# Kernel optimization log

Hardware: AMD Instinct MI355X
Metric: run time of the kernel (lower is better)

The kernel has to match this reference:

```python
import jax, jax.numpy as jnp
import numpy as np

N_ITER = 50  # entmax_bisect default number of bisection iterations
ALPHA_MIN = 1.001


def setup_inputs() -> dict:
    key = jax.random.key(0)
    k1, k2 = jax.random.split(key)
    B, S = 4096, 4096
    scores = jax.random.normal(k1, (B, S), dtype=jnp.float32)
    mask = jax.random.randint(k2, (B, S), 0, 2).astype(bool)  # True = keep
    alpha = jnp.array(1.5, dtype=jnp.float32)  # learned scalar parameter
    return {"scores": scores, "mask": mask, "alpha": alpha}


def _entmax_bisect(Xs, alpha, n_iter=N_ITER):
    """Xs: scores already multiplied by (alpha-1), masked positions = -inf.
    Bisection search for the threshold tau such that sum(clip(Xs-tau,0)^(1/(alpha-1))) = 1.
    """
    d = Xs.shape[-1]
    exp = 1.0 / (alpha - 1.0)

    def p_of(tau):  # elementwise (clip(Xs - tau, 0))**exp, grad-safe at 0
        z = Xs - tau
        z_safe = jnp.where(z > 0, z, 1.0)
        return jnp.where(z > 0, z_safe ** exp, 0.0)

    max_val = jnp.max(Xs, axis=-1, keepdims=True)
    tau_lo = max_val - 1.0                                   # _gp(1, alpha) = 1
    tau_hi = max_val - (1.0 / d) ** (alpha - 1.0)            # _gp(1/d, alpha)
    f_lo = jnp.sum(p_of(tau_lo), axis=-1, keepdims=True) - 1.0  # fixed across iterations
    dm0 = tau_hi - tau_lo
    p0 = p_of(tau_lo)

    def body(carry, _):
        tau_lo, dm, _p = carry
        dm = dm * 0.5
        tau_m = tau_lo + dm
        p_m = p_of(tau_m)
        f_m = jnp.sum(p_m, axis=-1, keepdims=True) - 1.0
        tau_lo = jnp.where(f_m * f_lo >= 0, tau_m, tau_lo)
        return (tau_lo, dm, p_m), None

    (_, _, p_m), _ = jax.lax.scan(body, (tau_lo, dm0, p0), None, length=n_iter)
    # ensure_sum_one=True in entmax_bisect
    return p_m / jnp.sum(p_m, axis=-1, keepdims=True)


def reference(scores, mask, alpha):
    alpha_c = jnp.maximum(alpha, ALPHA_MIN)  # torch clamps alpha.data to >= 1.001
    # replace_masked_values(scores, mask, -inf), then X * (alpha - 1)
    Xs = jnp.where(mask, scores * (alpha_c - 1.0), -jnp.inf)
    return _entmax_bisect(Xs, alpha_c)
```

## Files before the change

### kernel.cpp

```cpp
#include <hip/hip_runtime.h>

#define DLEN     4096
#define TPB      256
#define NWAVE    4
#define EPT      16
#define CAPW     1024
#define AS_MAX    6
#define NBISECT  31

typedef float floatx4 __attribute__((ext_vector_type(4)));

__device__ __forceinline__ int prefix_cnt(unsigned long long bm) {
    return __builtin_amdgcn_mbcnt_hi((unsigned)(bm >> 32),
           __builtin_amdgcn_mbcnt_lo((unsigned)bm, 0u));
}

__global__ __launch_bounds__(TPB, 8)
void entmax_kernel(const float* __restrict__ scores,
                   const int* __restrict__ mask,
                   const float* __restrict__ alpha_ptr,
                   float* __restrict__ out)
{
    __shared__ float sv[NWAVE][CAPW + 64];
    __shared__ int   wcnt[NWAVE];
    __shared__ float wred[NWAVE];

    const int tid  = threadIdx.x;
    const int w    = tid >> 6;
    const int lane = tid & 63;
    const int row  = blockIdx.x;

    const float NEG = -1e30f;

    const float alpha = fmaxf(alpha_ptr[0], 1.001f);
    const float am1   = alpha - 1.0f;
    const float expo  = 1.0f / am1;
    const bool  sq    = (expo == 2.0f);

    const size_t base = (size_t)row * DLEN;
    const float* srow = scores + base;
    const int*   mrow = mask + base;

    float xs[EPT];
    float wmax = NEG;
#pragma unroll
    for (int c = 0; c < 4; ++c) {
        const int idx = c * (TPB * 4) + tid * 4;
        const float4 s = *reinterpret_cast<const float4*>(srow + idx);
        const int4   m = *reinterpret_cast<const int4*>(mrow + idx);
        const float x0 = m.x ? s.x * am1 : NEG;
        const float x1 = m.y ? s.y * am1 : NEG;
        const float x2 = m.z ? s.z * am1 : NEG;
        const float x3 = m.w ? s.w * am1 : NEG;
        xs[c*4+0] = x0; xs[c*4+1] = x1; xs[c*4+2] = x2; xs[c*4+3] = x3;
        wmax = fmaxf(wmax, fmaxf(fmaxf(x0, x1), fmaxf(x2, x3)));
    }
#pragma unroll
    for (int off = 32; off; off >>= 1)
        wmax = fmaxf(wmax, __shfl_xor(wmax, off));
    if (lane == 0) wred[w] = wmax;
    __syncthreads();
    const float rmax = fmaxf(fmaxf(wred[0], wred[1]), fmaxf(wred[2], wred[3]));

    const float tau_lo0 = rmax - 1.0f;

    int cnt = 0;
#pragma unroll
    for (int e = 0; e < EPT; ++e) {
        const bool pred = xs[e] > tau_lo0;
        const unsigned long long bm = __ballot(pred);
        if (pred)
            sv[w][cnt + prefix_cnt(bm)] = xs[e];
        cnt += __popcll(bm);
    }
    sv[w][cnt + lane] = NEG;
    if (lane == 0) wcnt[w] = cnt;
    __syncthreads();

    int nct[NWAVE];
    bool fast = true;
#pragma unroll
    for (int ws = 0; ws < NWAVE; ++ws) {
        const int c4 = wcnt[ws];
        nct[ws] = (c4 + 63) >> 6;
        fast = fast && (c4 <= 64);
    }

    float tau_m = tau_lo0;
    float sum_m = 1.0f;

    if (sq) {
        float k_prev = -1.0f;
        if (fast) {
            const float r0 = sv[0][lane];
            const float r1 = sv[1][lane];
            const float r2 = sv[2][lane];
            const float r3 = sv[3][lane];
#pragma unroll 1
            for (int it = 0; it < AS_MAX; ++it) {
                const float z0 = fmaxf(r0 - tau_m, 0.f);
                const float z1 = fmaxf(r1 - tau_m, 0.f);
                const float z2 = fmaxf(r2 - tau_m, 0.f);
                const float z3 = fmaxf(r3 - tau_m, 0.f);
                float s2 = z0 * z0;
                s2 = fmaf(z1, z1, s2);
                s2 = fmaf(z2, z2, s2);
                s2 = fmaf(z3, z3, s2);
                float s1 = (z0 + z1) + (z2 + z3);
                float k  = ((z0 > 0.f ? 1.f : 0.f) + (z1 > 0.f ? 1.f : 0.f))
                         + ((z2 > 0.f ? 1.f : 0.f) + (z3 > 0.f ? 1.f : 0.f));
#pragma unroll
                for (int off = 32; off; off >>= 1) {
                    s2 += __shfl_xor(s2, off);
                    s1 += __shfl_xor(s1, off);
                    k  += __shfl_xor(k,  off);
                }
                sum_m = s2;
                if (k == k_prev || k <= 0.f) break;
                k_prev = k;
                const float disc = fmaxf(fmaf(-k, s2 - 1.0f, s1 * s1), 0.f);
                tau_m += (s1 - sqrtf(disc)) / k;
            }
        } else {
#pragma unroll 1
            for (int it = 0; it < AS_MAX; ++it) {
                float s2 = 0.f, s1 = 0.f, k = 0.f;
                for (int ws = 0; ws < NWAVE; ++ws) {
                    const int n = nct[ws];
                    for (int c = 0; c < n; ++c) {
                        const float z = fmaxf(sv[ws][c * 64 + lane] - tau_m, 0.f);
                        s2 = fmaf(z, z, s2);
                        s1 += z;
                        k  += (z > 0.f) ? 1.f : 0.f;
                    }
                }
#pragma unroll
                for (int off = 32; off; off >>= 1) {
                    s2 += __shfl_xor(s2, off);
                    s1 += __shfl_xor(s1, off);
                    k  += __shfl_xor(k,  off);
                }
                sum_m = s2;
                if (k == k_prev || k <= 0.f) break;
                k_prev = k;
                const float disc = fmaxf(fmaf(-k, s2 - 1.0f, s1 * s1), 0.f);
                tau_m += (s1 - sqrtf(disc)) / k;
            }
        }
    } else {
        const float tau_hi = rmax - exp2f(-12.0f * am1);

        auto rsum = [&](float tau) -> float {
            float s = 0.f;
            for (int ws = 0; ws < NWAVE; ++ws) {
                const int n = nct[ws];
                for (int c = 0; c < n; ++c) {
                    const float z = sv[ws][c * 64 + lane] - tau;
                    s += (z > 0.f) ? powf(z, expo) : 0.f;
                }
            }
#pragma unroll
            for (int off = 32; off; off >>= 1) s += __shfl_xor(s, off);
            return s;
        };

        float tau_lo = tau_lo0;
        const float f_lo = rsum(tau_lo0) - 1.0f;
        float dm = tau_hi - tau_lo0;
#pragma unroll 1
        for (int it = 0; it < NBISECT; ++it) {
            dm *= 0.5f;
            tau_m = tau_lo + dm;
            sum_m = rsum(tau_m);
            const float f_m = sum_m - 1.0f;
            tau_lo = (f_m * f_lo >= 0.0f) ? tau_m : tau_lo;
        }
    }

    const float inv = 1.0f / sum_m;
#pragma unroll
    for (int c = 0; c < 4; ++c) {
        const int idx = c * (TPB * 4) + tid * 4;
        floatx4 o;
        if (sq) {
            float z;
            z = fmaxf(xs[c*4+0] - tau_m, 0.f); o.x = z * z * inv;
            z = fmaxf(xs[c*4+1] - tau_m, 0.f); o.y = z * z * inv;
            z = fmaxf(xs[c*4+2] - tau_m, 0.f); o.z = z * z * inv;
            z = fmaxf(xs[c*4+3] - tau_m, 0.f); o.w = z * z * inv;
        } else {
            float z;
            z = xs[c*4+0] - tau_m; o.x = (z > 0.f) ? powf(z, expo) * inv : 0.f;
            z = xs[c*4+1] - tau_m; o.y = (z > 0.f) ? powf(z, expo) * inv : 0.f;
            z = xs[c*4+2] - tau_m; o.z = (z > 0.f) ? powf(z, expo) * inv : 0.f;
            z = xs[c*4+3] - tau_m; o.w = (z > 0.f) ? powf(z, expo) * inv : 0.f;
        }
        __builtin_nontemporal_store(o, reinterpret_cast<floatx4*>(out + base + idx));
    }
}

extern "C" void kernel_launch(void* const* d_in, const int* in_sizes, int n_in,
                              void* d_out, int out_size, void* d_ws, size_t ws_size,
                              hipStream_t stream) {
    const float* scores = (const float*)d_in[0];
    const int*   mask   = (const int*)d_in[1];
    const float* alpha  = (const float*)d_in[2];
    float*       out    = (float*)d_out;
    const int rows = in_sizes[0] / DLEN;
    entmax_kernel<<<rows, TPB, 0, stream>>>(scores, mask, alpha, out);
}
```

Before: 39.11 us.

## Process two rows per block and prefetch the next row during the solve

Each block now handles two consecutive rows. It issues the global loads for the next row's scores and mask into registers right after the compaction barrier, so they overlap the threshold solve and output store of the current row. The aim is to hide memory latency that was previously exposed at the start of each block. In exchange the grid is halved, which lowers parallelism across CUs, and the prefetch buffers raise register pressure under launch bounds of 8 blocks per CU. There is also a possible hazard on the shared buffers when the second row overwrites them.

```diff
diff --git a/kernel.cpp b/kernel.cpp
--- a/kernel.cpp
+++ b/kernel.cpp
@@ -3,6 +3,7 @@
 #define DLEN     4096
 #define TPB      256
 #define NWAVE    4
+#define RPB      2
 #define EPT      16
 #define CAPW     1024
 #define AS_MAX    6
@@ -19,7 +20,8 @@
 void entmax_kernel(const float* __restrict__ scores,
                    const int* __restrict__ mask,
                    const float* __restrict__ alpha_ptr,
-                   float* __restrict__ out)
+                   float* __restrict__ out,
+                   int rows)
 {
     __shared__ float sv[NWAVE][CAPW + 64];
     __shared__ int   wcnt[NWAVE];
@@ -28,7 +30,6 @@
     const int tid  = threadIdx.x;
     const int w    = tid >> 6;
     const int lane = tid & 63;
-    const int row  = blockIdx.x;
 
     const float NEG = -1e30f;
 
@@ -37,165 +38,194 @@
     const float expo  = 1.0f / am1;
     const bool  sq    = (expo == 2.0f);
 
-    const size_t base = (size_t)row * DLEN;
-    const float* srow = scores + base;
-    const int*   mrow = mask + base;
-
-    float xs[EPT];
-    float wmax = NEG;
-#pragma unroll
-    for (int c = 0; c < 4; ++c) {
-        const int idx = c * (TPB * 4) + tid * 4;
-        const float4 s = *reinterpret_cast<const float4*>(srow + idx);
-        const int4   m = *reinterpret_cast<const int4*>(mrow + idx);
-        const float x0 = m.x ? s.x * am1 : NEG;
-        const float x1 = m.y ? s.y * am1 : NEG;
-        const float x2 = m.z ? s.z * am1 : NEG;
-        const float x3 = m.w ? s.w * am1 : NEG;
-        xs[c*4+0] = x0; xs[c*4+1] = x1; xs[c*4+2] = x2; xs[c*4+3] = x3;
-        wmax = fmaxf(wmax, fmaxf(fmaxf(x0, x1), fmaxf(x2, x3)));
+    const int row0 = blockIdx.x * RPB;
+
+    float4 s_pf[4];
+    int4   m_pf[4];
+
+    {
+        const float* srow = scores + (size_t)row0 * DLEN;
+        const int*   mrow = mask   + (size_t)row0 * DLEN;
+#pragma unroll
+        for (int c = 0; c < 4; ++c) {
+            const int idx = c * (TPB * 4) + tid * 4;
+            s_pf[c] = *reinterpret_cast<const float4*>(srow + idx);
+            m_pf[c] = *reinterpret_cast<const int4*>(mrow + idx);
+        }
     }
-#pragma unroll
-    for (int off = 32; off; off >>= 1)
-        wmax = fmaxf(wmax, __shfl_xor(wmax, off));
-    if (lane == 0) wred[w] = wmax;
-    __syncthreads();
-    const float rmax = fmaxf(fmaxf(wred[0], wred[1]), fmaxf(wred[2], wred[3]));
-
-    const float tau_lo0 = rmax - 1.0f;
-
-    int cnt = 0;
-#pragma unroll
-    for (int e = 0; e < EPT; ++e) {
-        const bool pred = xs[e] > tau_lo0;
-        const unsigned long long bm = __ballot(pred);
-        if (pred)
-            sv[w][cnt + prefix_cnt(bm)] = xs[e];
-        cnt += __popcll(bm);
-    }
-    sv[w][cnt + lane] = NEG;
-    if (lane == 0) wcnt[w] = cnt;
-    __syncthreads();
-
-    int nct[NWAVE];
-    bool fast = true;
-#pragma unroll
-    for (int ws = 0; ws < NWAVE; ++ws) {
-        const int c4 = wcnt[ws];
-        nct[ws] = (c4 + 63) >> 6;
-        fast = fast && (c4 <= 64);
-    }
-
-    float tau_m = tau_lo0;
-    float sum_m = 1.0f;
-
-    if (sq) {
-        float k_prev = -1.0f;
-        if (fast) {
-            const float r0 = sv[0][lane];
-            const float r1 = sv[1][lane];
-            const float r2 = sv[2][lane];
-            const float r3 = sv[3][lane];
-#pragma unroll 1
-            for (int it = 0; it < AS_MAX; ++it) {
-                const float z0 = fmaxf(r0 - tau_m, 0.f);
-                const float z1 = fmaxf(r1 - tau_m, 0.f);
-                const float z2 = fmaxf(r2 - tau_m, 0.f);
-                const float z3 = fmaxf(r3 - tau_m, 0.f);
-                float s2 = z0 * z0;
-                s2 = fmaf(z1, z1, s2);
-                s2 = fmaf(z2, z2, s2);
-                s2 = fmaf(z3, z3, s2);
-                float s1 = (z0 + z1) + (z2 + z3);
-                float k  = ((z0 > 0.f ? 1.f : 0.f) + (z1 > 0.f ? 1.f : 0.f))
-                         + ((z2 > 0.f ? 1.f : 0.f) + (z3 > 0.f ? 1.f : 0.f));
-#pragma unroll
-                for (int off = 32; off; off >>= 1) {
-                    s2 += __shfl_xor(s2, off);
-                    s1 += __shfl_xor(s1, off);
-                    k  += __shfl_xor(k,  off);
+
+#pragma unroll 1
+    for (int r = 0; r < RPB; ++r) {
+        const int row = row0 + r;
+        if (row >= rows) break;
+        const size_t base = (size_t)row * DLEN;
+
+        float xs[EPT];
+        float wmax = NEG;
+#pragma unroll
+        for (int c = 0; c < 4; ++c) {
+            const float4 s = s_pf[c];
+            const int4   m = m_pf[c];
+            const float x0 = m.x ? s.x * am1 : NEG;
+            const float x1 = m.y ? s.y * am1 : NEG;
+            const float x2 = m.z ? s.z * am1 : NEG;
+            const float x3 = m.w ? s.w * am1 : NEG;
+            xs[c*4+0] = x0; xs[c*4+1] = x1; xs[c*4+2] = x2; xs[c*4+3] = x3;
+            wmax = fmaxf(wmax, fmaxf(fmaxf(x0, x1), fmaxf(x2, x3)));
+        }
+#pragma unroll
+        for (int off = 32; off; off >>= 1)
+            wmax = fmaxf(wmax, __shfl_xor(wmax, off));
+        if (lane == 0) wred[w] = wmax;
+        __syncthreads();
+        const float rmax = fmaxf(fmaxf(wred[0], wred[1]), fmaxf(wred[2], wred[3]));
+
+        const float tau_lo0 = rmax - 1.0f;
+
+        int cnt = 0;
+#pragma unroll
+        for (int e = 0; e < EPT; ++e) {
+            const bool pred = xs[e] > tau_lo0;
+            const unsigned long long bm = __ballot(pred);
+            if (pred)
+                sv[w][cnt + prefix_cnt(bm)] = xs[e];
+            cnt += __popcll(bm);
+        }
+        sv[w][cnt + lane] = NEG;
+        if (lane == 0) wcnt[w] = cnt;
+        __syncthreads();
+
+        if (r + 1 < RPB && row + 1 < rows) {
+            const float* srow = scores + (size_t)(row + 1) * DLEN;
+            const int*   mrow = mask   + (size_t)(row + 1) * DLEN;
+#pragma unroll
+            for (int c = 0; c < 4; ++c) {
+                const int idx = c * (TPB * 4) + tid * 4;
+                s_pf[c] = *reinterpret_cast<const float4*>(srow + idx);
+                m_pf[c] = *reinterpret_cast<const int4*>(mrow + idx);
+            }
+        }
+
+        int nct[NWAVE];
+        bool fast = true;
+#pragma unroll
+        for (int ws = 0; ws < NWAVE; ++ws) {
+            const int c4 = wcnt[ws];
+            nct[ws] = (c4 + 63) >> 6;
+            fast = fast && (c4 <= 64);
+        }
+
+        float tau_m = tau_lo0;
+        float sum_m = 1.0f;
+
+        if (sq) {
+            float k_prev = -1.0f;
+            if (fast) {
+                const float r0 = sv[0][lane];
+                const float r1 = sv[1][lane];
+                const float r2 = sv[2][lane];
+                const float r3 = sv[3][lane];
+#pragma unroll 1
+                for (int it = 0; it < AS_MAX; ++it) {
+                    const float z0 = fmaxf(r0 - tau_m, 0.f);
+                    const float z1 = fmaxf(r1 - tau_m, 0.f);
+                    const float z2 = fmaxf(r2 - tau_m, 0.f);
+                    const float z3 = fmaxf(r3 - tau_m, 0.f);
+                    float s2 = z0 * z0;
+                    s2 = fmaf(z1, z1, s2);
+                    s2 = fmaf(z2, z2, s2);
+                    s2 = fmaf(z3, z3, s2);
+                    float s1 = (z0 + z1) + (z2 + z3);
+                    float k  = ((z0 > 0.f ? 1.f : 0.f) + (z1 > 0.f ? 1.f : 0.f))
+                             + ((z2 > 0.f ? 1.f : 0.f) + (z3 > 0.f ? 1.f : 0.f));
+#pragma unroll
+                    for (int off = 32; off; off >>= 1) {
+                        s2 += __shfl_xor(s2, off);
+                        s1 += __shfl_xor(s1, off);
+                        k  += __shfl_xor(k,  off);
+                    }
+                    sum_m = s2;
+                    if (k == k_prev || k <= 0.f) break;
+                    k_prev = k;
+                    const float disc = fmaxf(fmaf(-k, s2 - 1.0f, s1 * s1), 0.f);
+                    tau_m += (s1 - sqrtf(disc)) / k;
                 }
-                sum_m = s2;
-                if (k == k_prev || k <= 0.f) break;
-                k_prev = k;
-                const float disc = fmaxf(fmaf(-k, s2 - 1.0f, s1 * s1), 0.f);
-                tau_m += (s1 - sqrtf(disc)) / k;
+            } else {
+#pragma unroll 1
+                for (int it = 0; it < AS_MAX; ++it) {
+                    float s2 = 0.f, s1 = 0.f, k = 0.f;
+                    for (int ws = 0; ws < NWAVE; ++ws) {
+                        const int n = nct[ws];
+                        for (int c = 0; c < n; ++c) {
+                            const float z = fmaxf(sv[ws][c * 64 + lane] - tau_m, 0.f);
+                            s2 = fmaf(z, z, s2);
+                            s1 += z;
+                            k  += (z > 0.f) ? 1.f : 0.f;
+                        }
+                    }
+#pragma unroll
+                    for (int off = 32; off; off >>= 1) {
+                        s2 += __shfl_xor(s2, off);
+                        s1 += __shfl_xor(s1, off);
+                        k  += __shfl_xor(k,  off);
+                    }
+                    sum_m = s2;
+                    if (k == k_prev || k <= 0.f) break;
+                    k_prev = k;
+                    const float disc = fmaxf(fmaf(-k, s2 - 1.0f, s1 * s1), 0.f);
+                    tau_m += (s1 - sqrtf(disc)) / k;
+                }
             }
         } else {
-#pragma unroll 1
-            for (int it = 0; it < AS_MAX; ++it) {
-                float s2 = 0.f, s1 = 0.f, k = 0.f;
+            const float tau_hi = rmax - exp2f(-12.0f * am1);
+
+            auto rsum = [&](float tau) -> float {
+                float s = 0.f;
                 for (int ws = 0; ws < NWAVE; ++ws) {
                     const int n = nct[ws];
                     for (int c = 0; c < n; ++c) {
-                        const float z = fmaxf(sv[ws][c * 64 + lane] - tau_m, 0.f);
-                        s2 = fmaf(z, z, s2);
-                        s1 += z;
-                        k  += (z > 0.f) ? 1.f : 0.f;
+                        const float z = sv[ws][c * 64 + lane] - tau;
+                        s += (z > 0.f) ? powf(z, expo) : 0.f;
                     }
                 }
 #pragma unroll
-                for (int off = 32; off; off >>= 1) {
-                    s2 += __shfl_xor(s2, off);
-                    s1 += __shfl_xor(s1, off);
-                    k  += __shfl_xor(k,  off);
-                }
-                sum_m = s2;
-                if (k == k_prev || k <= 0.f) break;
-                k_prev = k;
-                const float disc = fmaxf(fmaf(-k, s2 - 1.0f, s1 * s1), 0.f);
-                tau_m += (s1 - sqrtf(disc)) / k;
-            }
-        }
-    } else {
-        const float tau_hi = rmax - exp2f(-12.0f * am1);
-
-        auto rsum = [&](float tau) -> float {
-            float s = 0.f;
-            for (int ws = 0; ws < NWAVE; ++ws) {
-                const int n = nct[ws];
-                for (int c = 0; c < n; ++c) {
-                    const float z = sv[ws][c * 64 + lane] - tau;
-                    s += (z > 0.f) ? powf(z, expo) : 0.f;
-                }
-            }
-#pragma unroll
-            for (int off = 32; off; off >>= 1) s += __shfl_xor(s, off);
-            return s;
-        };
-
-        float tau_lo = tau_lo0;
-        const float f_lo = rsum(tau_lo0) - 1.0f;
-        float dm = tau_hi - tau_lo0;
-#pragma unroll 1
-        for (int it = 0; it < NBISECT; ++it) {
-            dm *= 0.5f;
-            tau_m = tau_lo + dm;
-            sum_m = rsum(tau_m);
-            const float f_m = sum_m - 1.0f;
-            tau_lo = (f_m * f_lo >= 0.0f) ? tau_m : tau_lo;
-        }
-    }
-
-    const float inv = 1.0f / sum_m;
-#pragma unroll
-    for (int c = 0; c < 4; ++c) {
-        const int idx = c * (TPB * 4) + tid * 4;
-        floatx4 o;
-        if (sq) {
-            float z;
-            z = fmaxf(xs[c*4+0] - tau_m, 0.f); o.x = z * z * inv;
-            z = fmaxf(xs[c*4+1] - tau_m, 0.f); o.y = z * z * inv;
-            z = fmaxf(xs[c*4+2] - tau_m, 0.f); o.z = z * z * inv;
-            z = fmaxf(xs[c*4+3] - tau_m, 0.f); o.w = z * z * inv;
-        } else {
-            float z;
-            z = xs[c*4+0] - tau_m; o.x = (z > 0.f) ? powf(z, expo) * inv : 0.f;
-            z = xs[c*4+1] - tau_m; o.y = (z > 0.f) ? powf(z, expo) * inv : 0.f;
-            z = xs[c*4+2] - tau_m; o.z = (z > 0.f) ? powf(z, expo) * inv : 0.f;
-            z = xs[c*4+3] - tau_m; o.w = (z > 0.f) ? powf(z, expo) * inv : 0.f;
-        }
-        __builtin_nontemporal_store(o, reinterpret_cast<floatx4*>(out + base + idx));
+                for (int off = 32; off; off >>= 1) s += __shfl_xor(s, off);
+                return s;
+            };
+
+            float tau_lo = tau_lo0;
+            const float f_lo = rsum(tau_lo0) - 1.0f;
+            float dm = tau_hi - tau_lo0;
+#pragma unroll 1
+            for (int it = 0; it < NBISECT; ++it) {
+                dm *= 0.5f;
+                tau_m = tau_lo + dm;
+                sum_m = rsum(tau_m);
+                const float f_m = sum_m - 1.0f;
+                tau_lo = (f_m * f_lo >= 0.0f) ? tau_m : tau_lo;
+            }
+        }
+
+        const float inv = 1.0f / sum_m;
+#pragma unroll
+        for (int c = 0; c < 4; ++c) {
+            const int idx = c * (TPB * 4) + tid * 4;
+            floatx4 o;
+            if (sq) {
+                float z;
+                z = fmaxf(xs[c*4+0] - tau_m, 0.f); o.x = z * z * inv;
+                z = fmaxf(xs[c*4+1] - tau_m, 0.f); o.y = z * z * inv;
+                z = fmaxf(xs[c*4+2] - tau_m, 0.f); o.z = z * z * inv;
+                z = fmaxf(xs[c*4+3] - tau_m, 0.f); o.w = z * z * inv;
+            } else {
+                float z;
+                z = xs[c*4+0] - tau_m; o.x = (z > 0.f) ? powf(z, expo) * inv : 0.f;
+                z = xs[c*4+1] - tau_m; o.y = (z > 0.f) ? powf(z, expo) * inv : 0.f;
+                z = xs[c*4+2] - tau_m; o.z = (z > 0.f) ? powf(z, expo) * inv : 0.f;
+                z = xs[c*4+3] - tau_m; o.w = (z > 0.f) ? powf(z, expo) * inv : 0.f;
+            }
+            __builtin_nontemporal_store(o, reinterpret_cast<floatx4*>(out + base + idx));
+        }
     }
 }
 
@@ -207,5 +237,6 @@
     const float* alpha  = (const float*)d_in[2];
     float*       out    = (float*)d_out;
     const int rows = in_sizes[0] / DLEN;
-    entmax_kernel<<<rows, TPB, 0, stream>>>(scores, mask, alpha, out);
+    const int grid = (rows + RPB - 1) / RPB;
+    entmax_kernel<<<grid, TPB, 0, stream>>>(scores, mask, alpha, out, rows);
 }
```

After: 81.07 us. 2.07x slower.
